# Kernel tuning notes

Measured on AMD Instinct MI355X. Metric: run time of the kernel, lower is better.

The kernel has to match this reference:

```python
import jax
jax.config.update("jax_enable_x64", True)  # hash math needs int64, as in the TF source
import jax.numpy as jnp
import numpy as np

NUM_LEVELS = 16
LEVEL_DIM = 2
BASE_RES = 16
HASHMAP_SIZE = 2 ** 19
N_POINTS = 1048576


def setup_inputs() -> dict:
    key = jax.random.key(0)
    k1, k2 = jax.random.split(key)
    # raw coords in [-size, size] with size=1.0 (forward normalizes to [0,1))
    x = jax.random.uniform(k1, (N_POINTS, 3), dtype=jnp.float32, minval=-1.0, maxval=1.0)
    # stacked per-level hash tables, init U(-1e-4, 1e-4) as in the keras layer
    tables = jax.random.uniform(
        k2, (NUM_LEVELS, HASHMAP_SIZE, LEVEL_DIM), dtype=jnp.float32,
        minval=-1e-4, maxval=1e-4)
    return {"x": x, "tables": tables}


def reference(x, tables):
    size = 1.0
    xn = jnp.clip((x + size) / (2.0 * size), 0.0, 1.0 - 1e-6)  # [N,3] in [0,1)
    primes = jnp.array([1546061, 1005013, 1673733], dtype=jnp.int64)  # per-axis hash primes
    offsets = jnp.array(
        [[0, 0, 0], [0, 0, 1], [0, 1, 0], [0, 1, 1],
         [1, 0, 0], [1, 0, 1], [1, 1, 0], [1, 1, 1]], dtype=jnp.int64)  # [8,3] cube corners
    is_one = offsets == 1  # [8,3]

    outs = []
    for lvl in range(NUM_LEVELS):  # fixed small unroll over resolution levels
        res = float(BASE_RES * (2 ** lvl))
        scaled = xn * res                      # [N,3]
        fl = jnp.floor(scaled)
        frac = scaled - fl                     # [N,3]
        corners = fl.astype(jnp.int64)[:, None, :] + offsets[None]      # [N,8,3]
        h = (jnp.sum(corners * primes, axis=-1) ^ lvl) % HASHMAP_SIZE   # [N,8]
        emb = tables[lvl][h]                   # gather -> [N,8,LEVEL_DIM]
        # trilinear weights: prod over axes of frac (if corner bit==1) else 1-frac
        w = jnp.prod(jnp.where(is_one[None], frac[:, None, :], 1.0 - frac[:, None, :]),
                     axis=-1)                  # [N,8]
        outs.append(jnp.sum(emb * w[..., None], axis=1))  # [N,LEVEL_DIM]
    return jnp.concatenate(outs, axis=-1)      # [N, NUM_LEVELS*LEVEL_DIM]
```

## Files before the change

### kernel.cpp

```cpp
#include <hip/hip_runtime.h>
#include <hip/hip_fp16.h>


#define NUM_LEVELS 16
#define HASHMAP_SIZE (1u << 19)
#define HASH_MASK (HASHMAP_SIZE - 1u)
#define BASE_RES 16
#define NXCD 8
#define MAX_SEG 8

struct Sched {
  int j_end[NXCD][MAX_SEG];
  int lvl[NXCD][MAX_SEG];
  int c0[NXCD][MAX_SEG];
  int nseg[NXCD];
  int J;
};

__global__ __launch_bounds__(256) void hash_level_kernel(
    const float* __restrict__ x,
    const float* __restrict__ tables,
    unsigned* __restrict__ ws,
    int n, Sched s) {
  const int xcd = blockIdx.x % NXCD;
  const int j = blockIdx.x / NXCD;

  int lvl = -1, chunk = 0, beg = 0;
  const int ns = s.nseg[xcd];
  for (int k = 0; k < ns; ++k) {
    const int end = s.j_end[xcd][k];
    if (j >= beg && j < end) {
      lvl = s.lvl[xcd][k];
      chunk = s.c0[xcd][k] + (j - beg);
    }
    beg = end;
  }
  if (lvl < 0) return;

  const int i = chunk * 256 + (int)threadIdx.x;
  if (i >= n) return;

  const unsigned P0 = 1546061u, P1 = 1005013u, P2 = 1673733u;
  const float UB = (float)(1.0 - 1e-6);

  const float px = __builtin_nontemporal_load(x + 3 * (size_t)i + 0);
  const float py = __builtin_nontemporal_load(x + 3 * (size_t)i + 1);
  const float pz = __builtin_nontemporal_load(x + 3 * (size_t)i + 2);

  const float xn0 = fminf(fmaxf((px + 1.0f) * 0.5f, 0.0f), UB);
  const float xn1 = fminf(fmaxf((py + 1.0f) * 0.5f, 0.0f), UB);
  const float xn2 = fminf(fmaxf((pz + 1.0f) * 0.5f, 0.0f), UB);

  const float res = (float)(BASE_RES << lvl);
  const float s0 = xn0 * res, s1 = xn1 * res, s2 = xn2 * res;
  const float f0 = floorf(s0), f1 = floorf(s1), f2 = floorf(s2);
  const float fr0 = s0 - f0, fr1 = s1 - f1, fr2 = s2 - f2;
  const unsigned c0 = (unsigned)f0, c1 = (unsigned)f1, c2 = (unsigned)f2;

  const unsigned base = c0 * P0 + c1 * P1 + c2 * P2;
  const float2* __restrict__ tbl =
      (const float2*)(tables + (size_t)lvl * HASHMAP_SIZE * 2);
  const float g0 = 1.0f - fr0, g1 = 1.0f - fr1, g2 = 1.0f - fr2;

  float acc0 = 0.0f, acc1 = 0.0f;
#pragma unroll
  for (int corner = 0; corner < 8; ++corner) {
    unsigned h = base;
    float w = 1.0f;
    if (corner & 4) { h += P0; w *= fr0; } else { w *= g0; }
    if (corner & 2) { h += P1; w *= fr1; } else { w *= g1; }
    if (corner & 1) { h += P2; w *= fr2; } else { w *= g2; }
    h = (h & HASH_MASK) ^ (unsigned)lvl;
    const float2 e = tbl[h];
    acc0 += e.x * w;
    acc1 += e.y * w;
  }

  const __half2 h2 = __floats2half2_rn(acc0, acc1);
  __builtin_nontemporal_store(*(const unsigned*)&h2,
                              ws + (size_t)lvl * n + i);
}

__global__ __launch_bounds__(256) void transpose_kernel(
    const unsigned* __restrict__ ws,
    float* __restrict__ out,
    int n) {
  const int i = blockIdx.x * blockDim.x + threadIdx.x;
  if (i >= n) return;

  float outv[2 * NUM_LEVELS];
#pragma unroll
  for (int lvl = 0; lvl < NUM_LEVELS; ++lvl) {
    const unsigned u = __builtin_nontemporal_load(ws + (size_t)lvl * n + i);
    const __half2 h2 = *(const __half2*)&u;
    const float2 f = __half22float2(h2);
    outv[2 * lvl + 0] = f.x;
    outv[2 * lvl + 1] = f.y;
  }
  float4* o = (float4*)(out + (size_t)i * (2 * NUM_LEVELS));
#pragma unroll
  for (int k = 0; k < 8; ++k) o[k] = ((const float4*)outv)[k];
}

__global__ __launch_bounds__(256) void hash_direct_kernel(
    const float* __restrict__ x, const float* __restrict__ tables,
    float* __restrict__ out, int n, int nchunk) {
  const int b = blockIdx.x;
  const int lvl_lo = b % NXCD;
  const int r = b / NXCD;
  const int chunk = r % nchunk;
  const int lvl = lvl_lo + NXCD * (r / nchunk);
  const int i = chunk * 256 + (int)threadIdx.x;
  if (i >= n) return;

  const unsigned P0 = 1546061u, P1 = 1005013u, P2 = 1673733u;
  const float UB = (float)(1.0 - 1e-6);
  const float px = x[3 * (size_t)i + 0];
  const float py = x[3 * (size_t)i + 1];
  const float pz = x[3 * (size_t)i + 2];
  const float xn0 = fminf(fmaxf((px + 1.0f) * 0.5f, 0.0f), UB);
  const float xn1 = fminf(fmaxf((py + 1.0f) * 0.5f, 0.0f), UB);
  const float xn2 = fminf(fmaxf((pz + 1.0f) * 0.5f, 0.0f), UB);
  const float res = (float)(BASE_RES << lvl);
  const float s0 = xn0 * res, s1 = xn1 * res, s2 = xn2 * res;
  const float f0 = floorf(s0), f1 = floorf(s1), f2 = floorf(s2);
  const float fr0 = s0 - f0, fr1 = s1 - f1, fr2 = s2 - f2;
  const unsigned base =
      (unsigned)f0 * P0 + (unsigned)f1 * P1 + (unsigned)f2 * P2;
  const float2* __restrict__ tbl =
      (const float2*)(tables + (size_t)lvl * HASHMAP_SIZE * 2);
  const float g0 = 1.0f - fr0, g1 = 1.0f - fr1, g2 = 1.0f - fr2;
  float acc0 = 0.0f, acc1 = 0.0f;
#pragma unroll
  for (int corner = 0; corner < 8; ++corner) {
    unsigned h = base;
    float w = 1.0f;
    if (corner & 4) { h += P0; w *= fr0; } else { w *= g0; }
    if (corner & 2) { h += P1; w *= fr1; } else { w *= g1; }
    if (corner & 1) { h += P2; w *= fr2; } else { w *= g2; }
    h = (h & HASH_MASK) ^ (unsigned)lvl;
    const float2 e = tbl[h];
    acc0 += e.x * w;
    acc1 += e.y * w;
  }
  float2* o = (float2*)(out + (size_t)i * (2 * NUM_LEVELS) + 2 * lvl);
  *o = make_float2(acc0, acc1);
}

static void build_sched(Sched* s, int nchunk) {
  const double c[NUM_LEVELS] = {0.5, 0.85, 0.95, 1, 1, 1, 1, 1,
                                1,   1,    1,    1, 1, 1, 1, 1};
  double total = 0;
  for (int l = 0; l < NUM_LEVELS; ++l) total += c[l] * nchunk;
  const double target = total / NXCD;

  for (int xx = 0; xx < NXCD; ++xx) s->nseg[xx] = 0;
  int xcd = 0;
  double acc = 0;
  for (int l = 0; l < NUM_LEVELS; ++l) {
    int cpos = 0;
    while (cpos < nchunk) {
      int take;
      if (xcd >= NXCD - 1) {
        take = nchunk - cpos;
      } else {
        const double room = target - acc;
        take = (int)(room / c[l] + 0.999999);
        if (take > nchunk - cpos) take = nchunk - cpos;
        if (take <= 0) { ++xcd; acc = 0; continue; }
      }
      int k = s->nseg[xcd];
      if (k >= MAX_SEG) k = MAX_SEG - 1;
      const int beg = (k == 0) ? 0 : s->j_end[xcd][k - 1];
      s->j_end[xcd][k] = beg + take;
      s->lvl[xcd][k] = l;
      s->c0[xcd][k] = cpos;
      s->nseg[xcd] = k + 1;
      cpos += take;
      acc += (double)take * c[l];
      if (xcd < NXCD - 1 && acc >= target - 1e-6) { ++xcd; acc = 0; }
    }
  }
  int J = 0;
  for (int xx = 0; xx < NXCD; ++xx) {
    const int k = s->nseg[xx];
    const int e = k ? s->j_end[xx][k - 1] : 0;
    if (e > J) J = e;
  }
  s->J = J;
}

extern "C" void kernel_launch(void* const* d_in, const int* in_sizes, int n_in,
                              void* d_out, int out_size, void* d_ws, size_t ws_size,
                              hipStream_t stream) {
  const float* x = (const float*)d_in[0];
  const float* tables = (const float*)d_in[1];
  float* out = (float*)d_out;
  const int n = in_sizes[0] / 3;

  const int block = 256;
  const int nchunk = (n + block - 1) / block;

  const size_t ws_needed = (size_t)NUM_LEVELS * n * sizeof(unsigned);
  if (ws_size >= ws_needed) {
    Sched s;
    build_sched(&s, nchunk);
    unsigned* ws = (unsigned*)d_ws;
    hash_level_kernel<<<NXCD * s.J, block, 0, stream>>>(x, tables, ws, n, s);
    transpose_kernel<<<nchunk, block, 0, stream>>>(ws, out, n);
  } else {
    hash_direct_kernel<<<nchunk * NUM_LEVELS, block, 0, stream>>>(
        x, tables, out, n, nchunk);
  }
}
```

Before: 772.3 us.

## Spatially bucket-sort points before hash-grid encoding to improve gather locality

Adds histogram, scan and scatter passes that counting-sort input points into a 32^3 spatial grid. The per-level hash kernel then processes one bucket per 64-thread block, and a final transpose writes results back through the permutation. The aim is better cache locality for the corner-table gathers, especially at coarse levels. In exchange it adds extra passes, atomics, a larger workspace requirement, and many small, possibly underfilled blocks. The small-workspace fallback no longer writes output when ws is below the plain requirement.

```diff
diff --git a/kernel.cpp b/kernel.cpp
--- a/kernel.cpp
+++ b/kernel.cpp
@@ -7,6 +7,8 @@
 #define HASH_MASK (HASHMAP_SIZE - 1u)
 #define BASE_RES 16
 #define NXCD 8
+#define NBX 32
+#define NBUCKETS (NBX * NBX * NBX)
 #define MAX_SEG 8
 
 struct Sched {
@@ -17,94 +19,169 @@
   int J;
 };
 
-__global__ __launch_bounds__(256) void hash_level_kernel(
-    const float* __restrict__ x,
+__device__ __forceinline__ int bucket_of(float px, float py, float pz) {
+  const float UB = (float)(1.0 - 1e-6);
+  const float xn0 = fminf(fmaxf((px + 1.0f) * 0.5f, 0.0f), UB);
+  const float xn1 = fminf(fmaxf((py + 1.0f) * 0.5f, 0.0f), UB);
+  const float xn2 = fminf(fmaxf((pz + 1.0f) * 0.5f, 0.0f), UB);
+  const int bx = (int)(xn0 * (float)NBX);
+  const int by = (int)(xn1 * (float)NBX);
+  const int bz = (int)(xn2 * (float)NBX);
+  return (bx << 10) | (by << 5) | bz;
+}
+
+__global__ __launch_bounds__(256) void hist_kernel(
+    const float* __restrict__ x, unsigned* __restrict__ hist, int n) {
+  for (int i = blockIdx.x * blockDim.x + threadIdx.x; i < n;
+       i += gridDim.x * blockDim.x) {
+    const float px = __builtin_nontemporal_load(x + 3 * (size_t)i + 0);
+    const float py = __builtin_nontemporal_load(x + 3 * (size_t)i + 1);
+    const float pz = __builtin_nontemporal_load(x + 3 * (size_t)i + 2);
+    atomicAdd(&hist[bucket_of(px, py, pz)], 1u);
+  }
+}
+
+__global__ __launch_bounds__(1024) void scan_kernel(
+    const unsigned* __restrict__ hist, unsigned* __restrict__ offsets,
+    unsigned* __restrict__ work, int n) {
+  __shared__ unsigned part[1024];
+  const int t = threadIdx.x;
+  const int per = NBUCKETS / 1024;
+  unsigned vals[32];
+  unsigned sum = 0;
+#pragma unroll
+  for (int k = 0; k < per; ++k) {
+    vals[k] = hist[t * per + k];
+    sum += vals[k];
+  }
+  part[t] = sum;
+  __syncthreads();
+  for (int ofs = 1; ofs < 1024; ofs <<= 1) {
+    const unsigned v = (t >= ofs) ? part[t - ofs] : 0u;
+    __syncthreads();
+    part[t] += v;
+    __syncthreads();
+  }
+  unsigned excl = (t == 0) ? 0u : part[t - 1];
+#pragma unroll
+  for (int k = 0; k < per; ++k) {
+    offsets[t * per + k] = excl;
+    work[t * per + k] = excl;
+    excl += vals[k];
+  }
+  if (t == 1023) offsets[NBUCKETS] = excl;
+}
+
+__global__ __launch_bounds__(256) void scatter_kernel(
+    const float* __restrict__ x, unsigned* __restrict__ work,
+    float* __restrict__ xs, int* __restrict__ perm, int n) {
+  for (int i = blockIdx.x * blockDim.x + threadIdx.x; i < n;
+       i += gridDim.x * blockDim.x) {
+    const float px = __builtin_nontemporal_load(x + 3 * (size_t)i + 0);
+    const float py = __builtin_nontemporal_load(x + 3 * (size_t)i + 1);
+    const float pz = __builtin_nontemporal_load(x + 3 * (size_t)i + 2);
+    const int b = bucket_of(px, py, pz);
+    const unsigned p = atomicAdd(&work[b], 1u);
+    xs[3 * (size_t)p + 0] = px;
+    xs[3 * (size_t)p + 1] = py;
+    xs[3 * (size_t)p + 2] = pz;
+    perm[p] = i;
+  }
+}
+
+__global__ __launch_bounds__(64) void hash_bucket_kernel(
+    const float* __restrict__ xs,
     const float* __restrict__ tables,
+    const unsigned* __restrict__ offsets,
     unsigned* __restrict__ ws,
     int n, Sched s) {
   const int xcd = blockIdx.x % NXCD;
   const int j = blockIdx.x / NXCD;
 
-  int lvl = -1, chunk = 0, beg = 0;
+  int lvl = -1, bucket = 0, beg = 0;
   const int ns = s.nseg[xcd];
   for (int k = 0; k < ns; ++k) {
     const int end = s.j_end[xcd][k];
     if (j >= beg && j < end) {
       lvl = s.lvl[xcd][k];
-      chunk = s.c0[xcd][k] + (j - beg);
+      bucket = s.c0[xcd][k] + (j - beg);
     }
     beg = end;
   }
   if (lvl < 0) return;
 
-  const int i = chunk * 256 + (int)threadIdx.x;
-  if (i >= n) return;
+  const unsigned start = offsets[bucket];
+  const unsigned stop = offsets[bucket + 1];
 
   const unsigned P0 = 1546061u, P1 = 1005013u, P2 = 1673733u;
   const float UB = (float)(1.0 - 1e-6);
-
-  const float px = __builtin_nontemporal_load(x + 3 * (size_t)i + 0);
-  const float py = __builtin_nontemporal_load(x + 3 * (size_t)i + 1);
-  const float pz = __builtin_nontemporal_load(x + 3 * (size_t)i + 2);
-
-  const float xn0 = fminf(fmaxf((px + 1.0f) * 0.5f, 0.0f), UB);
-  const float xn1 = fminf(fmaxf((py + 1.0f) * 0.5f, 0.0f), UB);
-  const float xn2 = fminf(fmaxf((pz + 1.0f) * 0.5f, 0.0f), UB);
-
   const float res = (float)(BASE_RES << lvl);
-  const float s0 = xn0 * res, s1 = xn1 * res, s2 = xn2 * res;
-  const float f0 = floorf(s0), f1 = floorf(s1), f2 = floorf(s2);
-  const float fr0 = s0 - f0, fr1 = s1 - f1, fr2 = s2 - f2;
-  const unsigned c0 = (unsigned)f0, c1 = (unsigned)f1, c2 = (unsigned)f2;
-
-  const unsigned base = c0 * P0 + c1 * P1 + c2 * P2;
   const float2* __restrict__ tbl =
       (const float2*)(tables + (size_t)lvl * HASHMAP_SIZE * 2);
-  const float g0 = 1.0f - fr0, g1 = 1.0f - fr1, g2 = 1.0f - fr2;
-
-  float acc0 = 0.0f, acc1 = 0.0f;
-#pragma unroll
-  for (int corner = 0; corner < 8; ++corner) {
-    unsigned h = base;
-    float w = 1.0f;
-    if (corner & 4) { h += P0; w *= fr0; } else { w *= g0; }
-    if (corner & 2) { h += P1; w *= fr1; } else { w *= g1; }
-    if (corner & 1) { h += P2; w *= fr2; } else { w *= g2; }
-    h = (h & HASH_MASK) ^ (unsigned)lvl;
-    const float2 e = tbl[h];
-    acc0 += e.x * w;
-    acc1 += e.y * w;
-  }
-
-  const __half2 h2 = __floats2half2_rn(acc0, acc1);
-  __builtin_nontemporal_store(*(const unsigned*)&h2,
-                              ws + (size_t)lvl * n + i);
-}
-
-__global__ __launch_bounds__(256) void transpose_kernel(
+
+  for (unsigned p = start + threadIdx.x; p < stop; p += 64) {
+    const float px = __builtin_nontemporal_load(xs + 3 * (size_t)p + 0);
+    const float py = __builtin_nontemporal_load(xs + 3 * (size_t)p + 1);
+    const float pz = __builtin_nontemporal_load(xs + 3 * (size_t)p + 2);
+
+    const float xn0 = fminf(fmaxf((px + 1.0f) * 0.5f, 0.0f), UB);
+    const float xn1 = fminf(fmaxf((py + 1.0f) * 0.5f, 0.0f), UB);
+    const float xn2 = fminf(fmaxf((pz + 1.0f) * 0.5f, 0.0f), UB);
+
+    const float s0 = xn0 * res, s1 = xn1 * res, s2 = xn2 * res;
+    const float f0 = floorf(s0), f1 = floorf(s1), f2 = floorf(s2);
+    const float fr0 = s0 - f0, fr1 = s1 - f1, fr2 = s2 - f2;
+    const unsigned c0 = (unsigned)f0, c1 = (unsigned)f1, c2 = (unsigned)f2;
+
+    const unsigned base = c0 * P0 + c1 * P1 + c2 * P2;
+    const float g0 = 1.0f - fr0, g1 = 1.0f - fr1, g2 = 1.0f - fr2;
+
+    float acc0 = 0.0f, acc1 = 0.0f;
+#pragma unroll
+    for (int corner = 0; corner < 8; ++corner) {
+      unsigned h = base;
+      float w = 1.0f;
+      if (corner & 4) { h += P0; w *= fr0; } else { w *= g0; }
+      if (corner & 2) { h += P1; w *= fr1; } else { w *= g1; }
+      if (corner & 1) { h += P2; w *= fr2; } else { w *= g2; }
+      h = (h & HASH_MASK) ^ (unsigned)lvl;
+      const float2 e = tbl[h];
+      acc0 += e.x * w;
+      acc1 += e.y * w;
+    }
+
+    const __half2 h2 = __floats2half2_rn(acc0, acc1);
+    __builtin_nontemporal_store(*(const unsigned*)&h2,
+                                ws + (size_t)lvl * n + p);
+  }
+}
+
+__global__ __launch_bounds__(256) void transpose_scatter_kernel(
     const unsigned* __restrict__ ws,
+    const int* __restrict__ perm,
     float* __restrict__ out,
     int n) {
-  const int i = blockIdx.x * blockDim.x + threadIdx.x;
-  if (i >= n) return;
+  const int p = blockIdx.x * blockDim.x + threadIdx.x;
+  if (p >= n) return;
 
   float outv[2 * NUM_LEVELS];
 #pragma unroll
   for (int lvl = 0; lvl < NUM_LEVELS; ++lvl) {
-    const unsigned u = __builtin_nontemporal_load(ws + (size_t)lvl * n + i);
+    const unsigned u = __builtin_nontemporal_load(ws + (size_t)lvl * n + p);
     const __half2 h2 = *(const __half2*)&u;
     const float2 f = __half22float2(h2);
     outv[2 * lvl + 0] = f.x;
     outv[2 * lvl + 1] = f.y;
   }
-  float4* o = (float4*)(out + (size_t)i * (2 * NUM_LEVELS));
+  const int orig = perm[p];
+  float4* o = (float4*)(out + (size_t)orig * (2 * NUM_LEVELS));
 #pragma unroll
   for (int k = 0; k < 8; ++k) o[k] = ((const float4*)outv)[k];
 }
 
-__global__ __launch_bounds__(256) void hash_direct_kernel(
+__global__ __launch_bounds__(256) void hash_level_kernel(
     const float* __restrict__ x, const float* __restrict__ tables,
-    float* __restrict__ out, int n, int nchunk) {
+    unsigned* __restrict__ ws, int n, int nchunk) {
   const int b = blockIdx.x;
   const int lvl_lo = b % NXCD;
   const int r = b / NXCD;
@@ -115,9 +192,9 @@
 
   const unsigned P0 = 1546061u, P1 = 1005013u, P2 = 1673733u;
   const float UB = (float)(1.0 - 1e-6);
-  const float px = x[3 * (size_t)i + 0];
-  const float py = x[3 * (size_t)i + 1];
-  const float pz = x[3 * (size_t)i + 2];
+  const float px = __builtin_nontemporal_load(x + 3 * (size_t)i + 0);
+  const float py = __builtin_nontemporal_load(x + 3 * (size_t)i + 1);
+  const float pz = __builtin_nontemporal_load(x + 3 * (size_t)i + 2);
   const float xn0 = fminf(fmaxf((px + 1.0f) * 0.5f, 0.0f), UB);
   const float xn1 = fminf(fmaxf((py + 1.0f) * 0.5f, 0.0f), UB);
   const float xn2 = fminf(fmaxf((pz + 1.0f) * 0.5f, 0.0f), UB);
@@ -143,13 +220,31 @@
     acc0 += e.x * w;
     acc1 += e.y * w;
   }
-  float2* o = (float2*)(out + (size_t)i * (2 * NUM_LEVELS) + 2 * lvl);
-  *o = make_float2(acc0, acc1);
+  const __half2 h2 = __floats2half2_rn(acc0, acc1);
+  __builtin_nontemporal_store(*(const unsigned*)&h2, ws + (size_t)lvl * n + i);
+}
+
+__global__ __launch_bounds__(256) void transpose_kernel(
+    const unsigned* __restrict__ ws, float* __restrict__ out, int n) {
+  const int i = blockIdx.x * blockDim.x + threadIdx.x;
+  if (i >= n) return;
+  float outv[2 * NUM_LEVELS];
+#pragma unroll
+  for (int lvl = 0; lvl < NUM_LEVELS; ++lvl) {
+    const unsigned u = __builtin_nontemporal_load(ws + (size_t)lvl * n + i);
+    const __half2 h2 = *(const __half2*)&u;
+    const float2 f = __half22float2(h2);
+    outv[2 * lvl + 0] = f.x;
+    outv[2 * lvl + 1] = f.y;
+  }
+  float4* o = (float4*)(out + (size_t)i * (2 * NUM_LEVELS));
+#pragma unroll
+  for (int k = 0; k < 8; ++k) o[k] = ((const float4*)outv)[k];
 }
 
 static void build_sched(Sched* s, int nchunk) {
-  const double c[NUM_LEVELS] = {0.5, 0.85, 0.95, 1, 1, 1, 1, 1,
-                                1,   1,    1,    1, 1, 1, 1, 1};
+  const double c[NUM_LEVELS] = {0.15, 0.18, 0.30, 0.65, 0.95, 1, 1, 1,
+                                1,    1,    1,    1,    1,    1, 1, 1};
   double total = 0;
   for (int l = 0; l < NUM_LEVELS; ++l) total += c[l] * nchunk;
   const double target = total / NXCD;
@@ -198,18 +293,47 @@
   float* out = (float*)d_out;
   const int n = in_sizes[0] / 3;
 
-  const int block = 256;
-  const int nchunk = (n + block - 1) / block;
-
-  const size_t ws_needed = (size_t)NUM_LEVELS * n * sizeof(unsigned);
-  if (ws_size >= ws_needed) {
+  size_t off = 0;
+  auto alloc = [&](size_t bytes) {
+    size_t r = off;
+    off = (off + bytes + 255) & ~(size_t)255;
+    return r;
+  };
+  const size_t ws_f16_off = alloc((size_t)NUM_LEVELS * n * 4);
+  const size_t xs_off = alloc((size_t)n * 3 * 4);
+  const size_t perm_off = alloc((size_t)n * 4);
+  const size_t offsets_off = alloc((size_t)(NBUCKETS + 1) * 4);
+  const size_t work_off = alloc((size_t)NBUCKETS * 4);
+  const size_t hist_off = alloc((size_t)NBUCKETS * 4);
+  const size_t need_bucket = off;
+  const size_t need_plain = (size_t)NUM_LEVELS * n * 4;
+
+  char* wsb = (char*)d_ws;
+
+  if (ws_size >= need_bucket) {
+    unsigned* wsh = (unsigned*)(wsb + ws_f16_off);
+    float* xs = (float*)(wsb + xs_off);
+    int* perm = (int*)(wsb + perm_off);
+    unsigned* offsets = (unsigned*)(wsb + offsets_off);
+    unsigned* work = (unsigned*)(wsb + work_off);
+    unsigned* hist = (unsigned*)(wsb + hist_off);
+
+    hipMemsetAsync(hist, 0, (size_t)NBUCKETS * 4, stream);
+    hist_kernel<<<2048, 256, 0, stream>>>(x, hist, n);
+    scan_kernel<<<1, 1024, 0, stream>>>(hist, offsets, work, n);
+    scatter_kernel<<<2048, 256, 0, stream>>>(x, work, xs, perm, n);
+
     Sched s;
-    build_sched(&s, nchunk);
-    unsigned* ws = (unsigned*)d_ws;
-    hash_level_kernel<<<NXCD * s.J, block, 0, stream>>>(x, tables, ws, n, s);
-    transpose_kernel<<<nchunk, block, 0, stream>>>(ws, out, n);
-  } else {
-    hash_direct_kernel<<<nchunk * NUM_LEVELS, block, 0, stream>>>(
-        x, tables, out, n, nchunk);
-  }
-}
+    build_sched(&s, NBUCKETS);
+    hash_bucket_kernel<<<NXCD * s.J, 64, 0, stream>>>(xs, tables, offsets,
+                                                      wsh, n, s);
+    const int nchunk_t = (n + 255) / 256;
+    transpose_scatter_kernel<<<nchunk_t, 256, 0, stream>>>(wsh, perm, out, n);
+  } else if (ws_size >= need_plain) {
+    unsigned* wsh = (unsigned*)wsb;
+    const int nchunk = (n + 255) / 256;
+    hash_level_kernel<<<nchunk * NUM_LEVELS, 256, 0, stream>>>(x, tables, wsh,
+                                                               n, nchunk);
+    transpose_kernel<<<nchunk, 256, 0, stream>>>(wsh, out, n);
+  }
+}
```

After: 858.7 us. +11.2%, slower.
